# Optimization experiments

Measured on AMD Instinct MI355X. Metric: run time of the kernel, lower is better.

Reference implementation:

```python
import jax, jax.numpy as jnp
import numpy as np
from jax import lax

B, C, N, NB = 64, 512, 1024, 4
BC = C // NB
KS = [3, 5, 7, 9]
LEVEL = 2  # min(2, pywt.dwt_max_level(1024, 8)) = 2
FL = 8  # db4 filter length
DN = ('NCH', 'OIH', 'NCH')
# pywt db4 decomposition filters
DEC_LO = jnp.array([-0.010597401784997278, 0.032883011666982945, 0.030841381835986965,
                    -0.18703481171888114, -0.02798376941698385, 0.6308807679295904,
                    0.7148465705525415, 0.23037781330885523], jnp.float32)
DEC_HI = jnp.array([-0.23037781330885523, 0.7148465705525415, -0.6308807679295904,
                    -0.02798376941698385, 0.18703481171888114, 0.030841381835986965,
                    -0.032883011666982945, -0.010597401784997278], jnp.float32)


def conv1d(x, w, b, pad):
    y = lax.conv_general_dilated(x, w, (1,), [(pad, pad)], dimension_numbers=DN)
    return y + b[None, :, None]


def bn_relu(x, g, beta, eps=1e-5):
    # BatchNorm1d in train mode: batch statistics over (B, L) per channel
    mu = x.mean(axis=(0, 2), keepdims=True)
    var = ((x - mu) ** 2).mean(axis=(0, 2), keepdims=True)
    xn = (x - mu) * lax.rsqrt(var + eps)
    return jax.nn.relu(xn * g[None, :, None] + beta[None, :, None])


def dwt1d(x):
    # single-level pywt-compatible DWT, symmetric mode. x: [B, C, n]
    b, c, n = x.shape
    out = (n + FL - 1) // 2
    p = 2 * (out - 1) - n + FL
    xp = jnp.pad(x, ((0, 0), (0, 0), (p // 2, p - p // 2)), mode='symmetric')
    k = jnp.stack([DEC_LO[::-1], DEC_HI[::-1]])[:, None, :]  # [2,1,FL]
    y = lax.conv_general_dilated(xp.reshape(b * c, 1, -1), k, (2,), 'VALID',
                                 dimension_numbers=DN)
    y = y.reshape(b, c, 2, out)
    return y[:, :, 0], y[:, :, 1]  # (cA, cD)


def idwt1d(lo, hi):
    # single-level inverse DWT; output length = 2*nc - FL + 2
    b, c, nc = lo.shape
    x = jnp.stack([lo, hi], axis=2).reshape(b * c, 2, nc)
    # rec filters = dec filters reversed, so flipped-for-conv == dec filters
    k = jnp.stack([DEC_LO, DEC_HI])[None, :, :]  # [1,2,FL]
    y = lax.conv_general_dilated(x, k, (1,), [(FL - 1, FL - 1)],
                                 lhs_dilation=(2,), dimension_numbers=DN)
    y = y[:, 0, FL - 2: FL - 2 + 2 * nc - FL + 2]
    return y.reshape(b, c, -1)


def decouple(x):
    # TemporalPatternDecoupling: db4 wavedec(level=2) -> reconstruct low-pass-only
    # (long term) and detail-only (short term). Torch detaches before pywt.
    x = lax.stop_gradient(x)
    n = x.shape[-1]
    a, details = x, []
    for _ in range(LEVEL):
        a, d = dwt1d(a)
        details.append(d)
    la, sa = a, jnp.zeros_like(a)
    for d in reversed(details):
        dl = d.shape[-1]
        la = idwt1d(la[..., :dl], jnp.zeros_like(d))
        sa = idwt1d(sa[..., :dl], d)
    return sa[..., :n], la[..., :n]


def setup_inputs() -> dict:
    key = jax.random.key(0)
    ks = jax.random.split(key, 32)
    s = 0.05
    inp = {
        'x': jax.random.normal(ks[0], (B, C, N), jnp.float32),
        'w_init': jax.random.normal(ks[1], (C, C, 1), jnp.float32) * s,
        'b_init': jnp.zeros((C,), jnp.float32),
        'w_pf': jax.random.normal(ks[2], (BC, 2 * BC, 1), jnp.float32) * s,
        'b_pf': jnp.zeros((BC,), jnp.float32),
        'w_fus': jax.random.normal(ks[3], (C, C, 1), jnp.float32) * s,
        'b_fus': jnp.zeros((C,), jnp.float32),
    }
    for i in range(NB):
        inp[f'w_b{i + 1}'] = jax.random.normal(ks[4 + i], (BC, BC, KS[i]), jnp.float32) * s
        inp[f'b_b{i + 1}'] = jnp.zeros((BC,), jnp.float32)
        inp[f'g_b{i + 1}'] = jnp.ones((BC,), jnp.float32)
        inp[f'be_b{i + 1}'] = jnp.zeros((BC,), jnp.float32)
    return inp


def reference(x, w_init, b_init, w_b1, b_b1, g_b1, be_b1, w_b2, b_b2, g_b2, be_b2,
              w_b3, b_b3, g_b3, be_b3, w_b4, b_b4, g_b4, be_b4, w_pf, b_pf,
              w_fus, b_fus):
    identity = x
    h = conv1d(x, w_init, b_init, 0)
    branch_in = jnp.split(h, NB, axis=1)
    wb = [w_b1, w_b2, w_b3, w_b4]
    bb = [b_b1, b_b2, b_b3, b_b4]
    gb = [g_b1, g_b2, g_b3, g_b4]
    beb = [be_b1, be_b2, be_b3, be_b4]
    shorts, longs = [], []
    for i in range(NB):
        y = bn_relu(conv1d(branch_in[i], wb[i], bb[i], KS[i] // 2), gb[i], beb[i])
        s, l = decouple(y)
        shorts.append(s)
        longs.append(l)
    for b in range(1, NB):
        shorts[b] = shorts[b] + shorts[b - 1]
    for b in range(NB - 2, -1, -1):
        longs[b] = longs[b] + longs[b + 1]
    enhanced = [conv1d(jnp.concatenate([shorts[b], longs[b]], axis=1), w_pf, b_pf, 0)
                for b in range(NB)]
    out = conv1d(jnp.concatenate(enhanced, axis=1), w_fus, b_fus, 0)
    return out + identity
```

## Files before the change

kernel.cpp:

```cpp
#include <hip/hip_runtime.h>

typedef float  f32x4 __attribute__((ext_vector_type(4)));
typedef short  s16x8 __attribute__((ext_vector_type(8)));
typedef short  s16x4 __attribute__((ext_vector_type(4)));
typedef unsigned short u16;

struct PtrQuad { const float* p[4]; };

__constant__ float c_lo[8] = {-0.010597401784997278f, 0.032883011666982945f,
                              0.030841381835986965f, -0.18703481171888114f,
                              -0.02798376941698385f, 0.6308807679295904f,
                              0.7148465705525415f,  0.23037781330885523f};
__constant__ float c_hi[8] = {-0.23037781330885523f, 0.7148465705525415f,
                              -0.6308807679295904f, -0.02798376941698385f,
                              0.18703481171888114f, 0.030841381835986965f,
                              -0.032883011666982945f, -0.010597401784997278f};

__device__ __forceinline__ u16 f2bf(float f) {
    unsigned u = __float_as_uint(f);
    u += 0x7fffu + ((u >> 16) & 1u);
    return (u16)(u >> 16);
}
__device__ __forceinline__ float bf2f(u16 h) {
    return __uint_as_float(((unsigned)h) << 16);
}
__device__ __forceinline__ int lds_chunk(int row, int g) {
    return row * 4 + (g ^ ((row >> 1) & 3));
}
__device__ __forceinline__ void gload16(void* lds, const void* g) {
    __builtin_amdgcn_global_load_lds(
        (__attribute__((address_space(1))) const void*)g,
        (__attribute__((address_space(3))) void*)lds,
        16, 0, 0);
}
__device__ __forceinline__ void pipe_wait(int t, int nt) {
    if (t + 2 < nt)      asm volatile("s_waitcnt vmcnt(8)" ::: "memory");
    else if (t + 1 < nt) asm volatile("s_waitcnt vmcnt(4)" ::: "memory");
    else                 asm volatile("s_waitcnt vmcnt(0)" ::: "memory");
    __builtin_amdgcn_s_barrier();
    __builtin_amdgcn_sched_barrier(0);
}
__device__ __forceinline__ void pipe_endbar() {
    __builtin_amdgcn_sched_barrier(0);
    __builtin_amdgcn_s_barrier();
}

__global__ __launch_bounds__(256) void gemm_nt_k(
    const u16* __restrict__ A, long aB, int lda,
    const u16* __restrict__ B, long bB, int ldb,
    int K,
    u16* __restrict__ D, long dB, int dj,
    const float* __restrict__ bias)
{
    __shared__ s16x8 As[3 * 512];
    __shared__ s16x8 Bs[3 * 512];
    int flat = blockIdx.x + 8 * (blockIdx.y + 4 * blockIdx.z);
    int swz = (flat & 7) * 256 + (flat >> 3);
    const int j0 = (swz & 7) * 128;
    const int i0 = ((swz >> 3) & 3) * 128;
    const long bb = swz >> 5;
    const u16* Ab = A + bb * aB;
    const u16* Bb = B + bb * bB;
    const int tid = threadIdx.x;
    const int srow = tid >> 2, sg = tid & 3;
    const int ssg = sg ^ ((srow >> 1) & 3);
    const int l = tid & 63, w = tid >> 6;
    const int wi = (w >> 1) * 64, wj = (w & 1) * 64;
    const int lr = l & 15, lg = l >> 4;
    const long aoff0 = (long)(i0 + srow) * lda + ssg * 8;
    const long aoff1 = (long)(i0 + srow + 64) * lda + ssg * 8;
    const long boff0 = (long)(j0 + srow) * ldb + ssg * 8;
    const long boff1 = (long)(j0 + srow + 64) * ldb + ssg * 8;
    const int nt = K >> 5;
    auto stage = [&](int buf, int t) {
        const int k0 = t << 5;
        char* a0 = (char*)As + buf * 8192 + w * 1024;
        char* b0 = (char*)Bs + buf * 8192 + w * 1024;
        gload16(a0, Ab + aoff0 + k0);
        gload16(a0 + 4096, Ab + aoff1 + k0);
        gload16(b0, Bb + boff0 + k0);
        gload16(b0 + 4096, Bb + boff1 + k0);
    };
    f32x4 acc[4][4] = {};
    stage(0, 0);
    if (nt > 1) stage(1, 1);
    int cur = 0;
    for (int t = 0; t < nt; ++t) {
        if (t + 2 < nt) stage((cur + 2) % 3, t + 2);
        pipe_wait(t, nt);
        s16x8 af[4], bf[4];
        #pragma unroll
        for (int f = 0; f < 4; ++f) {
            af[f] = As[cur * 512 + lds_chunk(wi + f * 16 + lr, lg)];
            bf[f] = Bs[cur * 512 + lds_chunk(wj + f * 16 + lr, lg)];
        }
        #pragma unroll
        for (int fi = 0; fi < 4; ++fi)
            #pragma unroll
            for (int fj = 0; fj < 4; ++fj)
                acc[fi][fj] = __builtin_amdgcn_mfma_f32_16x16x32_bf16(af[fi], bf[fj], acc[fi][fj], 0, 0, 0);
        pipe_endbar();
        cur = (cur + 1) % 3;
    }
    u16* Db = D + bb * dB;
    #pragma unroll
    for (int fi = 0; fi < 4; ++fi) {
        const int i = i0 + wi + fi * 16 + lg * 4;
        float b0 = 0, b1 = 0, b2v = 0, b3 = 0;
        if (bias) { b0 = bias[i]; b1 = bias[i + 1]; b2v = bias[i + 2]; b3 = bias[i + 3]; }
        #pragma unroll
        for (int fj = 0; fj < 4; ++fj) {
            const int j = j0 + wj + fj * 16 + lr;
            f32x4 d = acc[fi][fj];
            s16x4 o;
            o[0] = (short)f2bf(d[0] + b0); o[1] = (short)f2bf(d[1] + b1);
            o[2] = (short)f2bf(d[2] + b2v); o[3] = (short)f2bf(d[3] + b3);
            *(s16x4*)(Db + (long)j * dj + i) = o;
        }
    }
}

__global__ __launch_bounds__(256) void gemm_branch4_k(
    const u16* __restrict__ WpAll,
    const u16* __restrict__ H,
    u16* __restrict__ Y,
    const u16* __restrict__ zbuf,
    float* __restrict__ part)
{
    __shared__ s16x8 As[3 * 512];
    __shared__ s16x8 Bs[3 * 512];
    __shared__ float sred[2][128];
    __shared__ float qred[2][128];
    int flat = blockIdx.x + 8 * (blockIdx.y + 4 * blockIdx.z);
    int swz = (flat & 7) * 256 + (flat >> 3);
    const int jblk = swz & 7;
    const int br = (swz >> 3) & 3;
    const long bb = swz >> 5;
    const int j0 = jblk * 128;
    const int taps = 3 + 2 * br;
    const int pad = 1 + br;
    const u16* Wp = WpAll + (long)(br * br + 2 * br) * 16384;
    const u16* Hb = H + bb * 524288 + 128 * br;
    const int tid = threadIdx.x;
    const int srow = tid >> 2, sg = tid & 3;
    const int ssg = sg ^ ((srow >> 1) & 3);
    const int l = tid & 63, w = tid >> 6;
    const int wi = (w >> 1) * 64, wj = (w & 1) * 64;
    const int lr = l & 15, lg = l >> 4;
    const int lda = taps * 128;
    const int nt = taps * 4;
    auto stage = [&](int buf, int t) {
        const int k0 = t << 5;
        const int tap = k0 >> 7, kc = k0 & 127;
        const int shift = tap - pad;
        char* a0 = (char*)As + buf * 8192 + w * 1024;
        char* b0 = (char*)Bs + buf * 8192 + w * 1024;
        gload16(a0, Wp + (long)srow * lda + k0 + ssg * 8);
        gload16(a0 + 4096, Wp + (long)(srow + 64) * lda + k0 + ssg * 8);
        int n0r = j0 + srow + shift;
        int n1r = n0r + 64;
        const u16* s0 = (n0r >= 0 && n0r < 1024) ? (Hb + (long)n0r * 512 + kc + ssg * 8) : zbuf;
        const u16* s1 = (n1r >= 0 && n1r < 1024) ? (Hb + (long)n1r * 512 + kc + ssg * 8) : zbuf;
        gload16(b0, s0);
        gload16(b0 + 4096, s1);
    };
    f32x4 acc[4][4] = {};
    stage(0, 0);
    stage(1, 1);
    int cur = 0;
    for (int t = 0; t < nt; ++t) {
        if (t + 2 < nt) stage((cur + 2) % 3, t + 2);
        pipe_wait(t, nt);
        s16x8 af[4], bf[4];
        #pragma unroll
        for (int f = 0; f < 4; ++f) {
            af[f] = As[cur * 512 + lds_chunk(wi + f * 16 + lr, lg)];
            bf[f] = Bs[cur * 512 + lds_chunk(wj + f * 16 + lr, lg)];
        }
        #pragma unroll
        for (int fi = 0; fi < 4; ++fi)
            #pragma unroll
            for (int fj = 0; fj < 4; ++fj)
                acc[fi][fj] = __builtin_amdgcn_mfma_f32_16x16x32_bf16(af[fi], bf[fj], acc[fi][fj], 0, 0, 0);
        pipe_endbar();
        cur = (cur + 1) % 3;
    }
    u16* Db = Y + bb * 524288 + 128 * br;
    #pragma unroll
    for (int fi = 0; fi < 4; ++fi) {
        const int i = wi + fi * 16 + lg * 4;
        #pragma unroll
        for (int fj = 0; fj < 4; ++fj) {
            const int j = j0 + wj + fj * 16 + lr;
            f32x4 d = acc[fi][fj];
            s16x4 o;
            o[0] = (short)f2bf(d[0]); o[1] = (short)f2bf(d[1]);
            o[2] = (short)f2bf(d[2]); o[3] = (short)f2bf(d[3]);
            *(s16x4*)(Db + (long)j * 512 + i) = o;
        }
    }
    float sv[16], qv[16];
    #pragma unroll
    for (int fi = 0; fi < 4; ++fi)
        #pragma unroll
        for (int e = 0; e < 4; ++e) {
            float s = 0.f, q = 0.f;
            #pragma unroll
            for (int fj = 0; fj < 4; ++fj) { float d = acc[fi][fj][e]; s += d; q += d * d; }
            sv[fi * 4 + e] = s; qv[fi * 4 + e] = q;
        }
    #pragma unroll
    for (int m = 1; m < 16; m <<= 1) {
        #pragma unroll
        for (int r = 0; r < 16; ++r) {
            sv[r] += __shfl_xor(sv[r], m, 64);
            qv[r] += __shfl_xor(qv[r], m, 64);
        }
    }
    __syncthreads();
    if (lr == 0) {
        #pragma unroll
        for (int r = 0; r < 16; ++r) {
            int co = wi + (r >> 2) * 16 + lg * 4 + (r & 3);
            sred[w & 1][co] = sv[r];
            qred[w & 1][co] = qv[r];
        }
    }
    __syncthreads();
    if (tid < 128) {
        long blk = (long)br * 512 + bb * 8 + jblk;
        part[blk * 256 + tid]       = sred[0][tid] + sred[1][tid];
        part[blk * 256 + 128 + tid] = qred[0][tid] + qred[1][tid];
    }
}

__global__ __launch_bounds__(256) void gemm_psl_k(
    const u16* __restrict__ Ybn,
    const u16* __restrict__ Bmat,
    u16* __restrict__ PSL)
{
    __shared__ s16x8 As[3 * 512];
    __shared__ s16x8 Bs[3 * 512];
    int flat = blockIdx.x + 8 * (blockIdx.y + 8 * blockIdx.z);
    int swz = (flat & 7) * 512 + (flat >> 3);
    const int j0 = (swz & 7) * 128;
    const int i0 = ((swz >> 3) & 7) * 128;
    const long bb = swz >> 6;
    const int tid = threadIdx.x;
    const u16* Ab = Ybn + bb * 524288;
    const int srow = tid >> 2, sg = tid & 3;
    const int ssg = sg ^ ((srow >> 1) & 3);
    const int l = tid & 63, w = tid >> 6;
    const int wi = (w >> 1) * 64, wj = (w & 1) * 64;
    const int lr = l & 15, lg = l >> 4;
    const long aoff0 = (long)(i0 + srow) * 512 + ssg * 8;
    const long aoff1 = (long)(i0 + srow + 64) * 512 + ssg * 8;
    const long boff0 = (long)(j0 + srow) * 512 + ssg * 8;
    const long boff1 = (long)(j0 + srow + 64) * 512 + ssg * 8;
    const int nt = 16;
    auto stage = [&](int buf, int t) {
        const int k0 = t << 5;
        char* a0 = (char*)As + buf * 8192 + w * 1024;
        char* b0 = (char*)Bs + buf * 8192 + w * 1024;
        gload16(a0, Ab + aoff0 + k0);
        gload16(a0 + 4096, Ab + aoff1 + k0);
        gload16(b0, Bmat + boff0 + k0);
        gload16(b0 + 4096, Bmat + boff1 + k0);
    };
    f32x4 acc[4][4] = {};
    stage(0, 0);
    stage(1, 1);
    int cur = 0;
    for (int t = 0; t < nt; ++t) {
        if (t + 2 < nt) stage((cur + 2) % 3, t + 2);
        pipe_wait(t, nt);
        s16x8 af[4], bf[4];
        #pragma unroll
        for (int f = 0; f < 4; ++f) {
            af[f] = As[cur * 512 + lds_chunk(wi + f * 16 + lr, lg)];
            bf[f] = Bs[cur * 512 + lds_chunk(wj + f * 16 + lr, lg)];
        }
        #pragma unroll
        for (int fi = 0; fi < 4; ++fi)
            #pragma unroll
            for (int fj = 0; fj < 4; ++fj)
                acc[fi][fj] = __builtin_amdgcn_mfma_f32_16x16x32_bf16(af[fi], bf[fj], acc[fi][fj], 0, 0, 0);
        pipe_endbar();
        cur = (cur + 1) % 3;
    }
    u16* Db = PSL + bb * 1048576;
    #pragma unroll
    for (int fi = 0; fi < 4; ++fi) {
        const int i = i0 + wi + fi * 16 + lg * 4;
        #pragma unroll
        for (int fj = 0; fj < 4; ++fj) {
            const int j = j0 + wj + fj * 16 + lr;
            f32x4 d = acc[fi][fj];
            s16x4 o;
            o[0] = (short)f2bf(d[0]); o[1] = (short)f2bf(d[1]);
            o[2] = (short)f2bf(d[2]); o[3] = (short)f2bf(d[3]);
            *(s16x4*)(Db + (long)j * 1024 + i) = o;
        }
    }
}

__global__ __launch_bounds__(256) void gemm_time_k(
    const u16* __restrict__ MS, const u16* __restrict__ ML,
    const u16* __restrict__ PSL,
    const float* __restrict__ b2, const float* __restrict__ X,
    float* __restrict__ OUT)
{
    __shared__ s16x8 As[3 * 512];
    __shared__ s16x8 Bs[3 * 512];
    int flat = blockIdx.x + 4 * (blockIdx.y + 8 * blockIdx.z);
    int swz = (flat & 7) * 256 + (flat >> 3);
    const int j0 = (swz & 3) * 128;
    const int i0 = ((swz >> 2) & 7) * 128;
    const long bb = swz >> 5;
    const int tid = threadIdx.x;
    const int srow = tid >> 2, sg = tid & 3;
    const int ssg = sg ^ ((srow >> 1) & 3);
    const int l = tid & 63, w = tid >> 6;
    const int wi = (w >> 1) * 64, wj = (w & 1) * 64;
    const int lr = l & 15, lg = l >> 4;
    const int klo = (i0 - 32) > 0 ? (i0 - 32) : 0;
    const int khi = (i0 + 160) < 1024 ? (i0 + 160) : 1024;
    const int nk = (khi - klo) >> 5;
    const int nt = nk * 2;
    auto stage = [&](int buf, int t) {
        const int pass = (t >= nk) ? 1 : 0;
        const int k0 = klo + ((t - (pass ? nk : 0)) << 5);
        const u16* A = pass ? ML : MS;
        const u16* B = PSL + bb * 1048576 + (long)pass * 524288;
        char* a0 = (char*)As + buf * 8192 + w * 1024;
        char* b0 = (char*)Bs + buf * 8192 + w * 1024;
        gload16(a0, A + (long)(i0 + srow) * 1024 + k0 + ssg * 8);
        gload16(a0 + 4096, A + (long)(i0 + srow + 64) * 1024 + k0 + ssg * 8);
        gload16(b0, B + (long)(j0 + srow) * 1024 + k0 + ssg * 8);
        gload16(b0 + 4096, B + (long)(j0 + srow + 64) * 1024 + k0 + ssg * 8);
    };
    f32x4 acc[4][4] = {};
    stage(0, 0);
    stage(1, 1);
    int cur = 0;
    for (int t = 0; t < nt; ++t) {
        if (t + 2 < nt) stage((cur + 2) % 3, t + 2);
        pipe_wait(t, nt);
        s16x8 af[4], bf[4];
        #pragma unroll
        for (int f = 0; f < 4; ++f) {
            af[f] = As[cur * 512 + lds_chunk(wi + f * 16 + lr, lg)];
            bf[f] = Bs[cur * 512 + lds_chunk(wj + f * 16 + lr, lg)];
        }
        #pragma unroll
        for (int fi = 0; fi < 4; ++fi)
            #pragma unroll
            for (int fj = 0; fj < 4; ++fj)
                acc[fi][fj] = __builtin_amdgcn_mfma_f32_16x16x32_bf16(af[fi], bf[fj], acc[fi][fj], 0, 0, 0);
        pipe_endbar();
        cur = (cur + 1) % 3;
    }
    float* Ob = OUT + bb * 524288;
    const float* Xb = X + bb * 524288;
    #pragma unroll
    for (int fi = 0; fi < 4; ++fi) {
        const int i = i0 + wi + fi * 16 + lg * 4;
        #pragma unroll
        for (int fj = 0; fj < 4; ++fj) {
            const int j = j0 + wj + fj * 16 + lr;
            const long a = (long)j * 1024 + i;
            f32x4 d = acc[fi][fj];
            const float bj = b2[j];
            f32x4 xv = *(const f32x4*)(Xb + a);
            f32x4 o;
            o[0] = d[0] + bj + xv[0]; o[1] = d[1] + bj + xv[1];
            o[2] = d[2] + bj + xv[2]; o[3] = d[3] + bj + xv[3];
            *(f32x4*)(Ob + a) = o;
        }
    }
}

__global__ __launch_bounds__(256) void cast_bf_k(const float* __restrict__ s, u16* __restrict__ d, int n)
{
    int i = blockIdx.x * 256 + threadIdx.x;
    if (i < n) d[i] = f2bf(s[i]);
}

__global__ __launch_bounds__(256) void pack_wb2_k(const float* __restrict__ s, u16* __restrict__ d, int taps)
{
    int i = blockIdx.x * 256 + threadIdx.x;
    if (i >= taps * 16384) return;
    int stride = taps * 128;
    int co = i / stride;
    int rem = i - co * stride;
    int tap = rem >> 7, ci = rem & 127;
    d[i] = f2bf(s[(long)(co * 128 + ci) * taps + tap]);
}

__global__ __launch_bounds__(256) void make_Ucum_k(
    const float* __restrict__ wf, const float* __restrict__ wp,
    u16* __restrict__ USc, u16* __restrict__ ULc)
{
    int gid = blockIdx.x * 256 + threadIdx.x;
    int co = gid >> 7, cc = gid & 127;
    float us[4], ul[4];
    #pragma unroll
    for (int b = 0; b < 4; ++b) {
        float s = 0.f, t = 0.f;
        for (int q = 0; q < 128; ++q) {
            float f = wf[(long)co * 512 + b * 128 + q];
            s += f * wp[q * 256 + cc];
            t += f * wp[q * 256 + 128 + cc];
        }
        us[b] = s; ul[b] = t;
    }
    float suf = 0.f;
    for (int b = 3; b >= 0; --b) { suf += us[b]; USc[(long)co * 512 + b * 128 + cc] = f2bf(suf); }
    float pre = 0.f;
    for (int b = 0; b < 4; ++b) { pre += ul[b]; ULc[(long)co * 512 + b * 128 + cc] = f2bf(pre); }
}

__global__ __launch_bounds__(256) void make_bias2_k(
    const float* __restrict__ wf, const float* __restrict__ bpf,
    const float* __restrict__ bfus, float* __restrict__ b2)
{
    int co = blockIdx.x * 256 + threadIdx.x;
    if (co >= 512) return;
    float s = bfus[co];
    for (int j = 0; j < 512; ++j) s += wf[(long)co * 512 + j] * bpf[j & 127];
    b2[co] = s;
}

__global__ __launch_bounds__(256) void eye_k(float* __restrict__ I)
{
    int i = blockIdx.x * 256 + threadIdx.x;
    I[i] = ((i >> 10) == (i & 1023)) ? 1.0f : 0.0f;
}

__global__ __launch_bounds__(256) void zero_k(float* __restrict__ p, int n)
{
    int i = blockIdx.x * 256 + threadIdx.x;
    if (i < n) p[i] = 0.f;
}

__global__ __launch_bounds__(256) void dwt_k(
    const float* __restrict__ x, float* __restrict__ a, float* __restrict__ d,
    int n_in, int n_out)
{
    const int row = blockIdx.y;
    const int m = blockIdx.x * 256 + threadIdx.x;
    if (m >= n_out) return;
    const float* xr = x + (long)row * n_in;
    float sa = 0.f, sd = 0.f;
    #pragma unroll
    for (int j = 0; j < 8; ++j) {
        int t = 2 * m + 1 - j;
        t = (t < 0) ? (-t - 1) : t;
        t = (t >= n_in) ? (2 * n_in - 1 - t) : t;
        const float v = xr[t];
        sa += v * c_lo[j];
        sd += v * c_hi[j];
    }
    a[(long)row * n_out + m] = sa;
    d[(long)row * n_out + m] = sd;
}

__global__ __launch_bounds__(256) void idwt_k(
    const float* __restrict__ lo, const float* __restrict__ hi,
    float* __restrict__ z, int nc, int n_out, long zB, int zN)
{
    const int row = blockIdx.y;
    const int m = blockIdx.x * 256 + threadIdx.x;
    if (m >= n_out) return;
    const float* lor = lo ? lo + (long)row * nc : nullptr;
    const float* hir = hi ? hi + (long)row * nc : nullptr;
    float s = 0.f;
    #pragma unroll
    for (int k = 0; k < 8; ++k) {
        int t = m + k - 1;
        if (t & 1) continue;
        int j = t >> 1;
        if (j >= nc) continue;
        if (lor) s += c_lo[k] * lor[j];
        if (hir) s += c_hi[k] * hir[j];
    }
    z[(long)(row >> 7) * zB + (long)(row & 127) * zN + m] = s;
}

__global__ __launch_bounds__(256) void trM_k(
    const float* __restrict__ S, const float* __restrict__ L,
    u16* __restrict__ MS, u16* __restrict__ ML)
{
    __shared__ float sh[32][33];
    const float* src = blockIdx.z ? L : S;
    u16* dst = blockIdx.z ? ML : MS;
    const int n0 = blockIdx.x * 32, m0 = blockIdx.y * 32;
    const int tx = threadIdx.x, ty = threadIdx.y;
    #pragma unroll
    for (int k = 0; k < 4; ++k)
        sh[ty + 8 * k][tx] = src[(long)(m0 + ty + 8 * k) * 1024 + n0 + tx];
    __syncthreads();
    #pragma unroll
    for (int k = 0; k < 4; ++k)
        dst[(long)(n0 + ty + 8 * k) * 1024 + m0 + tx] = f2bf(sh[tx][ty + 8 * k]);
}

__global__ __launch_bounds__(256) void trX_k(const float* __restrict__ x, u16* __restrict__ xcl)
{
    __shared__ float sh[32][33];
    const int n0 = blockIdx.x * 32, c0 = blockIdx.y * 32;
    const long bb = blockIdx.z;
    const int tx = threadIdx.x, ty = threadIdx.y;
    const float* xb = x + bb * 524288;
    u16* ob = xcl + bb * 524288;
    #pragma unroll
    for (int k = 0; k < 4; ++k)
        sh[ty + 8 * k][tx] = xb[(long)(c0 + ty + 8 * k) * 1024 + n0 + tx];
    __syncthreads();
    #pragma unroll
    for (int k = 0; k < 4; ++k)
        ob[(long)(n0 + ty + 8 * k) * 512 + c0 + tx] = f2bf(sh[tx][ty + 8 * k]);
}

__global__ __launch_bounds__(256) void bn_coef_k(
    const float* __restrict__ part, PtrQuad g, PtrQuad be, float* __restrict__ scsh)
{
    int c = blockIdx.x * 256 + threadIdx.x;
    if (c >= 512) return;
    int br = c >> 7, cc = c & 127;
    const float* pb = part + (long)br * 131072;
    float s = 0.f, q = 0.f;
    for (int pidx = 0; pidx < 512; ++pidx) {
        s += pb[pidx * 256 + cc];
        q += pb[pidx * 256 + 128 + cc];
    }
    float mu = s * (1.0f / 65536.0f);
    float var = q * (1.0f / 65536.0f) - mu * mu;
    float sc = g.p[br][cc] * rsqrtf(var + 1e-5f);
    scsh[c] = sc;
    scsh[512 + c] = be.p[br][cc] - mu * sc;
}

__global__ __launch_bounds__(256) void bn_apply_k(
    u16* __restrict__ Y, const float* __restrict__ scsh)
{
    __shared__ float sc_[512];
    __shared__ float sh_[512];
    const int t = threadIdx.x;
    #pragma unroll
    for (int q = 0; q < 2; ++q) {
        sc_[t + q * 256] = scsh[t + q * 256];
        sh_[t + q * 256] = scsh[512 + t + q * 256];
    }
    __syncthreads();
    long gid = (long)blockIdx.x * 256 + t;
    long r = gid >> 6; int cg = (int)(gid & 63);
    u16* p = Y + r * 512 + cg * 8;
    s16x8 v = *(const s16x8*)p;
    #pragma unroll
    for (int e = 0; e < 8; ++e) {
        int c = cg * 8 + e;
        float f = bf2f((u16)v[e]) * sc_[c] + sh_[c];
        v[e] = (short)f2bf(f > 0.f ? f : 0.f);
    }
    *(s16x8*)p = v;
}

extern "C" void kernel_launch(void* const* d_in, const int* in_sizes, int n_in,
                              void* d_out, int out_size, void* d_ws, size_t ws_size,
                              hipStream_t stream)
{
    const float* x      = (const float*)d_in[0];
    const float* w_init = (const float*)d_in[1];
    const float* b_init = (const float*)d_in[2];
    const float* w_pf   = (const float*)d_in[3];
    const float* b_pf   = (const float*)d_in[4];
    const float* w_fus  = (const float*)d_in[5];
    const float* b_fus  = (const float*)d_in[6];
    const float *w_b[4];
    PtrQuad g, be;
    for (int i = 0; i < 4; ++i) {
        w_b[i]  = (const float*)d_in[7 + 4 * i];
        g.p[i]  = (const float*)d_in[9 + 4 * i];
        be.p[i] = (const float*)d_in[10 + 4 * i];
    }
    float* outf = (float*)d_out;

    char* p = (char*)d_ws;
    u16* xcl   = (u16*)p;  p += 67108864;
    u16* h     = (u16*)p;  p += 67108864;
    u16* Y     = (u16*)p;  p += 67108864;
    u16* PSL   = (u16*)p;  p += 134217728;
    u16* Wi    = (u16*)p;  p += 524288;
    u16* Wp    = (u16*)p;  p += 786432;
    u16* UScULc= (u16*)p;  p += 1048576;
    u16* MrowS = (u16*)p;  p += 2097152;
    u16* MrowL = (u16*)p;  p += 2097152;
    float* eye = (float*)p; p += 4194304;
    float* Sid = (float*)p; p += 4194304;
    float* Lid = (float*)p; p += 4194304;
    float* a1  = (float*)p; p += 2109440;
    float* d1  = (float*)p; p += 2109440;
    float* a2  = (float*)p; p += 1069056;
    float* d2  = (float*)p; p += 1069056;
    float* la1 = (float*)p; p += 2109440;
    float* sa1 = (float*)p; p += 2109440;
    float* b2  = (float*)p; p += 2048;
    float* zbuf= (float*)p; p += 256;
    float* scsh= (float*)p; p += 4096;
    float* part= (float*)p; p += 2097152;

    const int KS_[4] = {3, 5, 7, 9};
    const long wpOff[4] = {0, 3 * 16384L, 8 * 16384L, 15 * 16384L};

    cast_bf_k<<<1024, 256, 0, stream>>>(w_init, Wi, 262144);
    for (int br = 0; br < 4; ++br)
        pack_wb2_k<<<(KS_[br] * 16384 + 255) / 256, 256, 0, stream>>>(w_b[br], Wp + wpOff[br], KS_[br]);
    make_Ucum_k<<<256, 256, 0, stream>>>(w_fus, w_pf, UScULc, UScULc + 262144);
    make_bias2_k<<<2, 256, 0, stream>>>(w_fus, b_pf, b_fus, b2);

    eye_k<<<4096, 256, 0, stream>>>(eye);
    dwt_k<<<dim3(3, 1024), 256, 0, stream>>>(eye, a1, d1, 1024, 515);
    dwt_k<<<dim3(2, 1024), 256, 0, stream>>>(a1, a2, d2, 515, 261);
    idwt_k<<<dim3(3, 1024), 256, 0, stream>>>(a2, nullptr, la1, 261, 515, 65920, 515);
    idwt_k<<<dim3(3, 1024), 256, 0, stream>>>(nullptr, d2, sa1, 261, 515, 65920, 515);
    idwt_k<<<dim3(4, 1024), 256, 0, stream>>>(la1, nullptr, Lid, 515, 1024, 131072, 1024);
    idwt_k<<<dim3(4, 1024), 256, 0, stream>>>(sa1, d1, Sid, 515, 1024, 131072, 1024);
    trM_k<<<dim3(32, 32, 2), dim3(32, 8), 0, stream>>>(Sid, Lid, MrowS, MrowL);

    trX_k<<<dim3(32, 16, 64), dim3(32, 8), 0, stream>>>(x, xcl);

    gemm_nt_k<<<dim3(8, 4, 64), 256, 0, stream>>>(Wi, 0, 512, xcl, 524288, 512, 512,
                                                  h, 524288, 512, b_init);

    zero_k<<<1, 256, 0, stream>>>(zbuf, 64);
    gemm_branch4_k<<<dim3(8, 4, 64), 256, 0, stream>>>(Wp, h, Y, (const u16*)zbuf, part);

    bn_coef_k<<<2, 256, 0, stream>>>(part, g, be, scsh);
    bn_apply_k<<<16384, 256, 0, stream>>>(Y, scsh);

    gemm_psl_k<<<dim3(8, 8, 64), 256, 0, stream>>>(Y, UScULc, PSL);

    gemm_time_k<<<dim3(4, 8, 64), 256, 0, stream>>>(MrowS, MrowL, PSL, b2, x, outf);
}
```

Measured before the change: 539.4 us.

## Use S+L=I identity to halve time GEMM, fuse setup kernels, double-buffer pipelines

The identity decomposition S+L=I is used so only the short-term matrix multiply runs in the time GEMM: the channel mixing folds (Us−Ul) against S and adds Ul-projected data directly in the epilogue. This halves the K loop of the final GEMM. The DWT operator construction is replaced by one fused per-column kernel, and the weight packing launches are merged. All GEMMs switch from triple to double buffering, which frees LDS but leaves less prefetch depth. Computing Us−Ul in bf16 may change rounding slightly.

Result: faster. 503.7 us (-6.6%).

```diff
diff --git a/kernel.cpp b/kernel.cpp
--- a/kernel.cpp
+++ b/kernel.cpp
@@ -33,10 +33,9 @@
         (__attribute__((address_space(3))) void*)lds,
         16, 0, 0);
 }
-__device__ __forceinline__ void pipe_wait(int t, int nt) {
-    if (t + 2 < nt)      asm volatile("s_waitcnt vmcnt(8)" ::: "memory");
-    else if (t + 1 < nt) asm volatile("s_waitcnt vmcnt(4)" ::: "memory");
-    else                 asm volatile("s_waitcnt vmcnt(0)" ::: "memory");
+__device__ __forceinline__ void pipe_wait2(int t, int nt) {
+    if (t + 1 < nt) asm volatile("s_waitcnt vmcnt(4)" ::: "memory");
+    else            asm volatile("s_waitcnt vmcnt(0)" ::: "memory");
     __builtin_amdgcn_s_barrier();
     __builtin_amdgcn_sched_barrier(0);
 }
@@ -52,8 +51,8 @@
     u16* __restrict__ D, long dB, int dj,
     const float* __restrict__ bias)
 {
-    __shared__ s16x8 As[3 * 512];
-    __shared__ s16x8 Bs[3 * 512];
+    __shared__ s16x8 As[2 * 512];
+    __shared__ s16x8 Bs[2 * 512];
     int flat = blockIdx.x + 8 * (blockIdx.y + 4 * blockIdx.z);
     int swz = (flat & 7) * 256 + (flat >> 3);
     const int j0 = (swz & 7) * 128;
@@ -83,11 +82,10 @@
     };
     f32x4 acc[4][4] = {};
     stage(0, 0);
-    if (nt > 1) stage(1, 1);
-    int cur = 0;
     for (int t = 0; t < nt; ++t) {
-        if (t + 2 < nt) stage((cur + 2) % 3, t + 2);
-        pipe_wait(t, nt);
+        const int cur = t & 1;
+        if (t + 1 < nt) stage(cur ^ 1, t + 1);
+        pipe_wait2(t, nt);
         s16x8 af[4], bf[4];
         #pragma unroll
         for (int f = 0; f < 4; ++f) {
@@ -100,7 +98,6 @@
             for (int fj = 0; fj < 4; ++fj)
                 acc[fi][fj] = __builtin_amdgcn_mfma_f32_16x16x32_bf16(af[fi], bf[fj], acc[fi][fj], 0, 0, 0);
         pipe_endbar();
-        cur = (cur + 1) % 3;
     }
     u16* Db = D + bb * dB;
     #pragma unroll
@@ -127,8 +124,8 @@
     const u16* __restrict__ zbuf,
     float* __restrict__ part)
 {
-    __shared__ s16x8 As[3 * 512];
-    __shared__ s16x8 Bs[3 * 512];
+    __shared__ s16x8 As[2 * 512];
+    __shared__ s16x8 Bs[2 * 512];
     __shared__ float sred[2][128];
     __shared__ float qred[2][128];
     int flat = blockIdx.x + 8 * (blockIdx.y + 4 * blockIdx.z);
@@ -166,11 +163,10 @@
     };
     f32x4 acc[4][4] = {};
     stage(0, 0);
-    stage(1, 1);
-    int cur = 0;
     for (int t = 0; t < nt; ++t) {
-        if (t + 2 < nt) stage((cur + 2) % 3, t + 2);
-        pipe_wait(t, nt);
+        const int cur = t & 1;
+        if (t + 1 < nt) stage(cur ^ 1, t + 1);
+        pipe_wait2(t, nt);
         s16x8 af[4], bf[4];
         #pragma unroll
         for (int f = 0; f < 4; ++f) {
@@ -183,7 +179,6 @@
             for (int fj = 0; fj < 4; ++fj)
                 acc[fi][fj] = __builtin_amdgcn_mfma_f32_16x16x32_bf16(af[fi], bf[fj], acc[fi][fj], 0, 0, 0);
         pipe_endbar();
-        cur = (cur + 1) % 3;
     }
     u16* Db = Y + bb * 524288 + 128 * br;
     #pragma unroll
@@ -239,8 +234,8 @@
     const u16* __restrict__ Bmat,
     u16* __restrict__ PSL)
 {
-    __shared__ s16x8 As[3 * 512];
-    __shared__ s16x8 Bs[3 * 512];
+    __shared__ s16x8 As[2 * 512];
+    __shared__ s16x8 Bs[2 * 512];
     int flat = blockIdx.x + 8 * (blockIdx.y + 8 * blockIdx.z);
     int swz = (flat & 7) * 512 + (flat >> 3);
     const int j0 = (swz & 7) * 128;
@@ -269,11 +264,10 @@
     };
     f32x4 acc[4][4] = {};
     stage(0, 0);
-    stage(1, 1);
-    int cur = 0;
     for (int t = 0; t < nt; ++t) {
-        if (t + 2 < nt) stage((cur + 2) % 3, t + 2);
-        pipe_wait(t, nt);
+        const int cur = t & 1;
+        if (t + 1 < nt) stage(cur ^ 1, t + 1);
+        pipe_wait2(t, nt);
         s16x8 af[4], bf[4];
         #pragma unroll
         for (int f = 0; f < 4; ++f) {
@@ -286,7 +280,6 @@
             for (int fj = 0; fj < 4; ++fj)
                 acc[fi][fj] = __builtin_amdgcn_mfma_f32_16x16x32_bf16(af[fi], bf[fj], acc[fi][fj], 0, 0, 0);
         pipe_endbar();
-        cur = (cur + 1) % 3;
     }
     u16* Db = PSL + bb * 1048576;
     #pragma unroll
@@ -305,13 +298,13 @@
 }
 
 __global__ __launch_bounds__(256) void gemm_time_k(
-    const u16* __restrict__ MS, const u16* __restrict__ ML,
+    const u16* __restrict__ MS,
     const u16* __restrict__ PSL,
     const float* __restrict__ b2, const float* __restrict__ X,
     float* __restrict__ OUT)
 {
-    __shared__ s16x8 As[3 * 512];
-    __shared__ s16x8 Bs[3 * 512];
+    __shared__ s16x8 As[2 * 512];
+    __shared__ s16x8 Bs[2 * 512];
     int flat = blockIdx.x + 4 * (blockIdx.y + 8 * blockIdx.z);
     int swz = (flat & 7) * 256 + (flat >> 3);
     const int j0 = (swz & 3) * 128;
@@ -325,27 +318,23 @@
     const int lr = l & 15, lg = l >> 4;
     const int klo = (i0 - 32) > 0 ? (i0 - 32) : 0;
     const int khi = (i0 + 160) < 1024 ? (i0 + 160) : 1024;
-    const int nk = (khi - klo) >> 5;
-    const int nt = nk * 2;
+    const int nt = (khi - klo) >> 5;
+    const u16* B = PSL + bb * 1048576;
     auto stage = [&](int buf, int t) {
-        const int pass = (t >= nk) ? 1 : 0;
-        const int k0 = klo + ((t - (pass ? nk : 0)) << 5);
-        const u16* A = pass ? ML : MS;
-        const u16* B = PSL + bb * 1048576 + (long)pass * 524288;
+        const int k0 = klo + (t << 5);
         char* a0 = (char*)As + buf * 8192 + w * 1024;
         char* b0 = (char*)Bs + buf * 8192 + w * 1024;
-        gload16(a0, A + (long)(i0 + srow) * 1024 + k0 + ssg * 8);
-        gload16(a0 + 4096, A + (long)(i0 + srow + 64) * 1024 + k0 + ssg * 8);
+        gload16(a0, MS + (long)(i0 + srow) * 1024 + k0 + ssg * 8);
+        gload16(a0 + 4096, MS + (long)(i0 + srow + 64) * 1024 + k0 + ssg * 8);
         gload16(b0, B + (long)(j0 + srow) * 1024 + k0 + ssg * 8);
         gload16(b0 + 4096, B + (long)(j0 + srow + 64) * 1024 + k0 + ssg * 8);
     };
     f32x4 acc[4][4] = {};
     stage(0, 0);
-    stage(1, 1);
-    int cur = 0;
     for (int t = 0; t < nt; ++t) {
-        if (t + 2 < nt) stage((cur + 2) % 3, t + 2);
-        pipe_wait(t, nt);
+        const int cur = t & 1;
+        if (t + 1 < nt) stage(cur ^ 1, t + 1);
+        pipe_wait2(t, nt);
         s16x8 af[4], bf[4];
         #pragma unroll
         for (int f = 0; f < 4; ++f) {
@@ -358,10 +347,10 @@
             for (int fj = 0; fj < 4; ++fj)
                 acc[fi][fj] = __builtin_amdgcn_mfma_f32_16x16x32_bf16(af[fi], bf[fj], acc[fi][fj], 0, 0, 0);
         pipe_endbar();
-        cur = (cur + 1) % 3;
     }
     float* Ob = OUT + bb * 524288;
     const float* Xb = X + bb * 524288;
+    const u16* PLb = PSL + bb * 1048576 + 524288;
     #pragma unroll
     for (int fi = 0; fi < 4; ++fi) {
         const int i = i0 + wi + fi * 16 + lg * 4;
@@ -372,34 +361,101 @@
             f32x4 d = acc[fi][fj];
             const float bj = b2[j];
             f32x4 xv = *(const f32x4*)(Xb + a);
+            s16x4 pl4 = *(const s16x4*)(PLb + a);
             f32x4 o;
-            o[0] = d[0] + bj + xv[0]; o[1] = d[1] + bj + xv[1];
-            o[2] = d[2] + bj + xv[2]; o[3] = d[3] + bj + xv[3];
+            o[0] = d[0] + bj + xv[0] + bf2f((u16)pl4[0]);
+            o[1] = d[1] + bj + xv[1] + bf2f((u16)pl4[1]);
+            o[2] = d[2] + bj + xv[2] + bf2f((u16)pl4[2]);
+            o[3] = d[3] + bj + xv[3] + bf2f((u16)pl4[3]);
             *(f32x4*)(Ob + a) = o;
         }
     }
 }
 
-__global__ __launch_bounds__(256) void cast_bf_k(const float* __restrict__ s, u16* __restrict__ d, int n)
+__global__ __launch_bounds__(256) void build_M_k(u16* __restrict__ MS)
+{
+    __shared__ float a1[515], d1[515], a2[261], d2[261], sa1[515];
+    const int r = blockIdx.x;
+    const int t = threadIdx.x;
+    for (int m = t; m < 515; m += 256) {
+        float sa = 0.f, sd = 0.f;
+        #pragma unroll
+        for (int j = 0; j < 8; ++j) {
+            int tt = 2 * m + 1 - j;
+            tt = (tt < 0) ? (-tt - 1) : tt;
+            tt = (tt >= 1024) ? (2047 - tt) : tt;
+            if (tt == r) { sa += c_lo[j]; sd += c_hi[j]; }
+        }
+        a1[m] = sa; d1[m] = sd;
+    }
+    __syncthreads();
+    for (int m = t; m < 261; m += 256) {
+        float sa = 0.f, sd = 0.f;
+        #pragma unroll
+        for (int j = 0; j < 8; ++j) {
+            int tt = 2 * m + 1 - j;
+            tt = (tt < 0) ? (-tt - 1) : tt;
+            tt = (tt >= 515) ? (1029 - tt) : tt;
+            float v = a1[tt];
+            sa += v * c_lo[j]; sd += v * c_hi[j];
+        }
+        a2[m] = sa; d2[m] = sd;
+    }
+    __syncthreads();
+    for (int m = t; m < 515; m += 256) {
+        float ss = 0.f;
+        #pragma unroll
+        for (int k = 0; k < 8; ++k) {
+            int tt = m + k - 1;
+            if (tt & 1) continue;
+            int j = tt >> 1;
+            if (j < 0 || j >= 261) continue;
+            ss += c_hi[k] * d2[j];
+        }
+        sa1[m] = ss;
+    }
+    __syncthreads();
+    for (int n = t; n < 1024; n += 256) {
+        float ss = 0.f;
+        #pragma unroll
+        for (int k = 0; k < 8; ++k) {
+            int tt = n + k - 1;
+            if (tt & 1) continue;
+            int j = tt >> 1;
+            if (j < 0 || j >= 515) continue;
+            ss += c_lo[k] * sa1[j] + c_hi[k] * d1[j];
+        }
+        MS[(long)n * 1024 + r] = f2bf(ss);
+    }
+}
+
+__global__ __launch_bounds__(256) void pack_weights_k(
+    const float* __restrict__ wi,
+    const float* __restrict__ b1, const float* __restrict__ b2_,
+    const float* __restrict__ b3, const float* __restrict__ b4,
+    u16* __restrict__ Wi, u16* __restrict__ Wp)
 {
     int i = blockIdx.x * 256 + threadIdx.x;
-    if (i < n) d[i] = f2bf(s[i]);
-}
-
-__global__ __launch_bounds__(256) void pack_wb2_k(const float* __restrict__ s, u16* __restrict__ d, int taps)
-{
-    int i = blockIdx.x * 256 + threadIdx.x;
-    if (i >= taps * 16384) return;
-    int stride = taps * 128;
-    int co = i / stride;
-    int rem = i - co * stride;
-    int tap = rem >> 7, ci = rem & 127;
-    d[i] = f2bf(s[(long)(co * 128 + ci) * taps + tap]);
+    if (i < 262144) Wi[i] = f2bf(wi[i]);
+    if (i < 393216) {
+        int base, taps;
+        const float* s;
+        if (i < 49152)       { base = 0;      taps = 3; s = b1; }
+        else if (i < 131072) { base = 49152;  taps = 5; s = b2_; }
+        else if (i < 245760) { base = 131072; taps = 7; s = b3; }
+        else                 { base = 245760; taps = 9; s = b4; }
+        int rem = i - base;
+        int stride = taps * 128;
+        int co = rem / stride;
+        int r2 = rem - co * stride;
+        int tap = r2 >> 7, ci = r2 & 127;
+        Wp[i] = f2bf(s[(long)(co * 128 + ci) * taps + tap]);
+    }
 }
 
 __global__ __launch_bounds__(256) void make_Ucum_k(
     const float* __restrict__ wf, const float* __restrict__ wp,
-    u16* __restrict__ USc, u16* __restrict__ ULc)
+    u16* __restrict__ UDUL)
 {
     int gid = blockIdx.x * 256 + threadIdx.x;
     int co = gid >> 7, cc = gid & 127;
@@ -414,10 +470,16 @@
         }
         us[b] = s; ul[b] = t;
     }
-    float suf = 0.f;
-    for (int b = 3; b >= 0; --b) { suf += us[b]; USc[(long)co * 512 + b * 128 + cc] = f2bf(suf); }
-    float pre = 0.f;
-    for (int b = 0; b < 4; ++b) { pre += ul[b]; ULc[(long)co * 512 + b * 128 + cc] = f2bf(pre); }
+    float suf[4], pre[4];
+    float acc = 0.f;
+    for (int b = 3; b >= 0; --b) { acc += us[b]; suf[b] = acc; }
+    acc = 0.f;
+    for (int b = 0; b < 4; ++b) { acc += ul[b]; pre[b] = acc; }
+    #pragma unroll
+    for (int b = 0; b < 4; ++b) {
+        UDUL[(long)co * 512 + b * 128 + cc]         = f2bf(suf[b] - pre[b]);
+        UDUL[(long)(512 + co) * 512 + b * 128 + cc] = f2bf(pre[b]);
+    }
 }
 
 __global__ __launch_bounds__(256) void make_bias2_k(
@@ -431,78 +493,10 @@
     b2[co] = s;
 }
 
-__global__ __launch_bounds__(256) void eye_k(float* __restrict__ I)
-{
-    int i = blockIdx.x * 256 + threadIdx.x;
-    I[i] = ((i >> 10) == (i & 1023)) ? 1.0f : 0.0f;
-}
-
 __global__ __launch_bounds__(256) void zero_k(float* __restrict__ p, int n)
 {
     int i = blockIdx.x * 256 + threadIdx.x;
     if (i < n) p[i] = 0.f;
-}
-
-__global__ __launch_bounds__(256) void dwt_k(
-    const float* __restrict__ x, float* __restrict__ a, float* __restrict__ d,
-    int n_in, int n_out)
-{
-    const int row = blockIdx.y;
-    const int m = blockIdx.x * 256 + threadIdx.x;
-    if (m >= n_out) return;
-    const float* xr = x + (long)row * n_in;
-    float sa = 0.f, sd = 0.f;
-    #pragma unroll
-    for (int j = 0; j < 8; ++j) {
-        int t = 2 * m + 1 - j;
-        t = (t < 0) ? (-t - 1) : t;
-        t = (t >= n_in) ? (2 * n_in - 1 - t) : t;
-        const float v = xr[t];
-        sa += v * c_lo[j];
-        sd += v * c_hi[j];
-    }
-    a[(long)row * n_out + m] = sa;
-    d[(long)row * n_out + m] = sd;
-}
-
-__global__ __launch_bounds__(256) void idwt_k(
-    const float* __restrict__ lo, const float* __restrict__ hi,
-    float* __restrict__ z, int nc, int n_out, long zB, int zN)
-{
-    const int row = blockIdx.y;
-    const int m = blockIdx.x * 256 + threadIdx.x;
-    if (m >= n_out) return;
-    const float* lor = lo ? lo + (long)row * nc : nullptr;
-    const float* hir = hi ? hi + (long)row * nc : nullptr;
-    float s = 0.f;
-    #pragma unroll
-    for (int k = 0; k < 8; ++k) {
-        int t = m + k - 1;
-        if (t & 1) continue;
-        int j = t >> 1;
-        if (j >= nc) continue;
-        if (lor) s += c_lo[k] * lor[j];
-        if (hir) s += c_hi[k] * hir[j];
-    }
-    z[(long)(row >> 7) * zB + (long)(row & 127) * zN + m] = s;
-}
-
-__global__ __launch_bounds__(256) void trM_k(
-    const float* __restrict__ S, const float* __restrict__ L,
-    u16* __restrict__ MS, u16* __restrict__ ML)
-{
-    __shared__ float sh[32][33];
-    const float* src = blockIdx.z ? L : S;
-    u16* dst = blockIdx.z ? ML : MS;
-    const int n0 = blockIdx.x * 32, m0 = blockIdx.y * 32;
-    const int tx = threadIdx.x, ty = threadIdx.y;
-    #pragma unroll
-    for (int k = 0; k < 4; ++k)
-        sh[ty + 8 * k][tx] = src[(long)(m0 + ty + 8 * k) * 1024 + n0 + tx];
-    __syncthreads();
-    #pragma unroll
-    for (int k = 0; k < 4; ++k)
-        dst[(long)(n0 + ty + 8 * k) * 1024 + m0 + tx] = f2bf(sh[tx][ty + 8 * k]);
 }
 
 __global__ __launch_bounds__(256) void trX_k(const float* __restrict__ x, u16* __restrict__ xcl)
@@ -593,53 +587,30 @@
     u16* PSL   = (u16*)p;  p += 134217728;
     u16* Wi    = (u16*)p;  p += 524288;
     u16* Wp    = (u16*)p;  p += 786432;
-    u16* UScULc= (u16*)p;  p += 1048576;
+    u16* UDUL  = (u16*)p;  p += 1048576;
     u16* MrowS = (u16*)p;  p += 2097152;
-    u16* MrowL = (u16*)p;  p += 2097152;
-    float* eye = (float*)p; p += 4194304;
-    float* Sid = (float*)p; p += 4194304;
-    float* Lid = (float*)p; p += 4194304;
-    float* a1  = (float*)p; p += 2109440;
-    float* d1  = (float*)p; p += 2109440;
-    float* a2  = (float*)p; p += 1069056;
-    float* d2  = (float*)p; p += 1069056;
-    float* la1 = (float*)p; p += 2109440;
-    float* sa1 = (float*)p; p += 2109440;
     float* b2  = (float*)p; p += 2048;
     float* zbuf= (float*)p; p += 256;
     float* scsh= (float*)p; p += 4096;
     float* part= (float*)p; p += 2097152;
 
-    const int KS_[4] = {3, 5, 7, 9};
-    const long wpOff[4] = {0, 3 * 16384L, 8 * 16384L, 15 * 16384L};
-
-    cast_bf_k<<<1024, 256, 0, stream>>>(w_init, Wi, 262144);
-    for (int br = 0; br < 4; ++br)
-        pack_wb2_k<<<(KS_[br] * 16384 + 255) / 256, 256, 0, stream>>>(w_b[br], Wp + wpOff[br], KS_[br]);
-    make_Ucum_k<<<256, 256, 0, stream>>>(w_fus, w_pf, UScULc, UScULc + 262144);
+    pack_weights_k<<<1536, 256, 0, stream>>>(w_init, w_b[0], w_b[1], w_b[2], w_b[3], Wi, Wp);
+    make_Ucum_k<<<256, 256, 0, stream>>>(w_fus, w_pf, UDUL);
     make_bias2_k<<<2, 256, 0, stream>>>(w_fus, b_pf, b_fus, b2);
-
-    eye_k<<<4096, 256, 0, stream>>>(eye);
-    dwt_k<<<dim3(3, 1024), 256, 0, stream>>>(eye, a1, d1, 1024, 515);
-    dwt_k<<<dim3(2, 1024), 256, 0, stream>>>(a1, a2, d2, 515, 261);
-    idwt_k<<<dim3(3, 1024), 256, 0, stream>>>(a2, nullptr, la1, 261, 515, 65920, 515);
-    idwt_k<<<dim3(3, 1024), 256, 0, stream>>>(nullptr, d2, sa1, 261, 515, 65920, 515);
-    idwt_k<<<dim3(4, 1024), 256, 0, stream>>>(la1, nullptr, Lid, 515, 1024, 131072, 1024);
-    idwt_k<<<dim3(4, 1024), 256, 0, stream>>>(sa1, d1, Sid, 515, 1024, 131072, 1024);
-    trM_k<<<dim3(32, 32, 2), dim3(32, 8), 0, stream>>>(Sid, Lid, MrowS, MrowL);
+    build_M_k<<<1024, 256, 0, stream>>>(MrowS);
+    zero_k<<<1, 256, 0, stream>>>(zbuf, 64);
 
     trX_k<<<dim3(32, 16, 64), dim3(32, 8), 0, stream>>>(x, xcl);
 
     gemm_nt_k<<<dim3(8, 4, 64), 256, 0, stream>>>(Wi, 0, 512, xcl, 524288, 512, 512,
                                                   h, 524288, 512, b_init);
 
-    zero_k<<<1, 256, 0, stream>>>(zbuf, 64);
     gemm_branch4_k<<<dim3(8, 4, 64), 256, 0, stream>>>(Wp, h, Y, (const u16*)zbuf, part);
 
     bn_coef_k<<<2, 256, 0, stream>>>(part, g, be, scsh);
     bn_apply_k<<<16384, 256, 0, stream>>>(Y, scsh);
 
-    gemm_psl_k<<<dim3(8, 8, 64), 256, 0, stream>>>(Y, UScULc, PSL);
-
-    gemm_time_k<<<dim3(4, 8, 64), 256, 0, stream>>>(MrowS, MrowL, PSL, b2, x, outf);
-}
+    gemm_psl_k<<<dim3(8, 8, 64), 256, 0, stream>>>(Y, UDUL, PSL);
+
+    gemm_time_k<<<dim3(4, 8, 64), 256, 0, stream>>>(MrowS, PSL, b2, x, outf);
+}
```
